# Kernel tuning notes

Hardware: AMD Instinct MI355X
Metric: run time of the kernel (lower is better)

Reference implementation:

```python
import jax, jax.numpy as jnp
import numpy as np

C = 256; G = 16; GC = C // G; K = 3; P = K * K
N = 4; H = 64; W = 64
PAD = 1; OFFSET_SCALE = 1.0; LN_EPS = 1e-5


def setup_inputs() -> dict:
    key = jax.random.key(0)
    ks = jax.random.split(key, 8)
    s = 0.02
    return {
        "x": jax.random.normal(ks[0], (N, C, H, W), jnp.float32),
        "dw_w": jax.random.normal(ks[1], (C, 1, K, K), jnp.float32) * s,
        "dw_b": jnp.zeros((C,), jnp.float32),
        "ln_g": jnp.ones((C,), jnp.float32),
        "ln_b": jnp.zeros((C,), jnp.float32),
        "off_w": jax.random.normal(ks[2], (C, G * P * 2), jnp.float32) * s,
        "off_b": jnp.zeros((G * P * 2,), jnp.float32),
        "mask_w": jax.random.normal(ks[3], (C, G * P), jnp.float32) * s,
        "mask_b": jnp.zeros((G * P,), jnp.float32),
        "inp_w": jax.random.normal(ks[4], (C, C), jnp.float32) * s,
        "inp_b": jnp.zeros((C,), jnp.float32),
        "out_w": jax.random.normal(ks[5], (C, C), jnp.float32) * s,
        "out_b": jnp.zeros((C,), jnp.float32),
    }


def _dcnv3_nchw(x, dw_w, dw_b, ln_g, ln_b, off_w, off_b, mask_w, mask_b,
                inp_w, inp_b, out_w, out_b):
    # NCHW -> NHWC (wrapper permute)
    xn = jnp.transpose(x, (0, 2, 3, 1))                      # (N,H,W,C)
    x_proj = xn @ inp_w + inp_b                              # input_proj

    # offset/mask branch: depthwise conv (NCHW) -> LayerNorm (channels-last) -> GELU
    x1 = jax.lax.conv_general_dilated(
        x, dw_w, window_strides=(1, 1), padding=((PAD, PAD), (PAD, PAD)),
        dimension_numbers=("NCHW", "OIHW", "NCHW"), feature_group_count=C)
    x1 = jnp.transpose(x1, (0, 2, 3, 1)) + dw_b
    mu = x1.mean(-1, keepdims=True)
    var = ((x1 - mu) ** 2).mean(-1, keepdims=True)
    x1 = (x1 - mu) * jax.lax.rsqrt(var + LN_EPS) * ln_g + ln_b
    x1 = jax.nn.gelu(x1, approximate=False)

    offset = (x1 @ off_w + off_b).reshape(N, H, W, G, P, 2)  # (x,y) pairs
    mask = jax.nn.softmax((x1 @ mask_w + mask_b).reshape(N, H, W, G, P), axis=-1)

    # pad sampled feature map with zeros (F.pad before sampling)
    xp = jnp.pad(x_proj, ((0, 0), (PAD, PAD), (PAD, PAD), (0, 0)))
    Hin, Win = H + 2 * PAD, W + 2 * PAD
    xg = xp.reshape(N, Hin, Win, G, GC)

    # reference points, normalized by padded size
    ref_y = (jnp.arange(H, dtype=jnp.float32) + PAD + 0.5) / Hin
    ref_x = (jnp.arange(W, dtype=jnp.float32) + PAD + 0.5) / Win
    ref = jnp.stack([jnp.broadcast_to(ref_x[None, :], (H, W)),
                     jnp.broadcast_to(ref_y[:, None], (H, W))], -1)  # (H,W,2)

    # dilation grid: x varies in the outer loop (torch meshgrid 'ij')
    d = jnp.arange(K, dtype=jnp.float32) - (K - 1) // 2     # [-1,0,1]
    gx = jnp.repeat(d, K) / Win
    gy = jnp.tile(d, K) / Hin
    grid = jnp.stack([gx, gy], -1)                           # (P,2)

    norm = jnp.array([Win, Hin], jnp.float32)
    loc = (ref[None, :, :, None, None, :] + grid * OFFSET_SCALE
           + offset * OFFSET_SCALE / norm)                   # (N,H,W,G,P,2)

    # grid_sample bilinear, align_corners=False, zero padding
    px = loc[..., 0] * Win - 0.5
    py = loc[..., 1] * Hin - 0.5
    x0 = jnp.floor(px); y0 = jnp.floor(py)
    wx = px - x0; wy = py - y0
    x0i = x0.astype(jnp.int32); y0i = y0.astype(jnp.int32)

    n_idx = jnp.arange(N)[:, None, None, None, None]
    g_idx = jnp.arange(G)[None, None, None, :, None]

    def corner(iy, ix, w):
        valid = (iy >= 0) & (iy < Hin) & (ix >= 0) & (ix < Win)
        v = xg[n_idx, jnp.clip(iy, 0, Hin - 1), jnp.clip(ix, 0, Win - 1), g_idx]
        wgt = jnp.where(valid, w, 0.0) * mask                # fold mask into weights
        return jnp.einsum("nhwgp,nhwgpc->nhwgc", wgt, v)

    out = (corner(y0i, x0i, (1 - wy) * (1 - wx))
           + corner(y0i, x0i + 1, (1 - wy) * wx)
           + corner(y0i + 1, x0i, wy * (1 - wx))
           + corner(y0i + 1, x0i + 1, wy * wx))               # (N,H,W,G,GC)

    out = out.reshape(N, H, W, C) @ out_w + out_b            # output_proj
    return jnp.transpose(out, (0, 3, 1, 2))                  # NHWC -> NCHW


def reference(x, dw_w, dw_b, ln_g, ln_b, off_w, off_b, mask_w, mask_b,
              inp_w, inp_b, out_w, out_b):
    return _dcnv3_nchw(x, dw_w, dw_b, ln_g, ln_b, off_w, off_b,
                       mask_w, mask_b, inp_w, inp_b, out_w, out_b)
```

## Files before the change

kernel.cpp:

```cpp
#include <hip/hip_runtime.h>
#include <hip/hip_bf16.h>
#include <math.h>


using bf16x8 = __attribute__((ext_vector_type(8))) short;
using f32x4  = __attribute__((ext_vector_type(4))) float;

#define GLOBAL_AS __attribute__((address_space(1)))
#define LDS_AS    __attribute__((address_space(3)))

static __device__ inline void g2lds16(const void* g, void* l) {
  __builtin_amdgcn_global_load_lds((const GLOBAL_AS int*)g, (LDS_AS int*)l, 16, 0, 0);
}
static __device__ inline unsigned short f2bf(float v) {
  __hip_bfloat16 b = __float2bfloat16(v);
  return *reinterpret_cast<unsigned short*>(&b);
}
static __device__ inline float us2f(unsigned short u) {
  union { unsigned u; float f; } c; c.u = ((unsigned)u) << 16; return c.f;
}

__global__ __launch_bounds__(256) void prep_k(
    const float* __restrict__ inp_w, const float* __restrict__ off_w,
    const float* __restrict__ off_b, const float* __restrict__ mask_w,
    const float* __restrict__ mask_b, const float* __restrict__ out_w,
    __hip_bfloat16* __restrict__ BtI, __hip_bfloat16* __restrict__ BtOM,
    __hip_bfloat16* __restrict__ BtO, float* __restrict__ bOM)
{
  int b = blockIdx.x, t = threadIdx.x;
  if (b < 256) {
    int n = b;
    BtI[n * 256 + t] = __float2bfloat16(inp_w[t * 256 + n]);
  } else if (b < 768) {
    int n = b - 256;
    float v = 0.f;
    if (n < 288) v = off_w[t * 288 + n];
    else if (n < 432) v = mask_w[t * 144 + (n - 288)];
    BtOM[n * 256 + t] = __float2bfloat16(v);
    if (b == 256) {
      for (int idx = t; idx < 512; idx += 256) {
        float bv = (idx < 288) ? off_b[idx] : ((idx < 432) ? mask_b[idx - 288] : 0.f);
        bOM[idx] = bv;
      }
    }
  } else {
    int n = b - 768;
    BtO[n * 256 + t] = __float2bfloat16(out_w[t * 256 + n]);
  }
}

__global__ __launch_bounds__(1024) void stage2_k(
    const float* __restrict__ x,
    const float* __restrict__ dw_w, const float* __restrict__ dw_b,
    const float* __restrict__ ln_g, const float* __restrict__ ln_b,
    const __hip_bfloat16* __restrict__ BtI, const float* __restrict__ inp_b,
    const __hip_bfloat16* __restrict__ BtOM, const float* __restrict__ bOM,
    __hip_bfloat16* __restrict__ xpu, __hip_bfloat16* __restrict__ om)
{
  __shared__ __align__(16) char smem[65152];
  unsigned short* x1t = (unsigned short*)smem;
  unsigned short* xs  = (unsigned short*)(smem + 33792);
  short* BsI  = (short*)(smem + 33792 + 13824);
  float* wgt  = (float*)(smem + 64000);
  float* psq  = (float*)(smem + 33792);
  float* murs = (float*)(smem + 64000);
  short* BsOM = (short*)(smem + 33792);

  const int blk = blockIdx.x;
  const int n4 = blk >> 6, h = blk & 63;
  const int t = threadIdx.x;
  const int w = t & 63, q = t >> 6;

  const int wave = t >> 6, lane = t & 63;
  const int quad = lane >> 4, lr = lane & 15;
  const int wm = wave >> 2, wn = wave & 3;

  f32x4 acc_i[4];
  #pragma unroll
  for (int i = 0; i < 4; ++i) acc_i[i] = (f32x4){0.f, 0.f, 0.f, 0.f};

  float s1 = 0.f, s2 = 0.f;
  for (int chunk = 0; chunk < 8; ++chunk) {
    const int ch0 = chunk * 32;
    if (t < 768) {
      int seg = t >> 3, part = t & 7;
      int r = seg >> 5, c = seg & 31;
      int px0 = part * 8;
      int hh = h + r - 1;
      float4 v0 = {0,0,0,0}, v1 = {0,0,0,0};
      if ((unsigned)hh < 64u) {
        const float* src = x + (size_t)n4 * 1048576 + (size_t)(ch0 + c) * 4096 + hh * 64 + px0;
        v0 = *(const float4*)src;
        v1 = *(const float4*)(src + 4);
      }
      uint4 u;
      u.x = (unsigned)f2bf(v0.x) | ((unsigned)f2bf(v0.y) << 16);
      u.y = (unsigned)f2bf(v0.z) | ((unsigned)f2bf(v0.w) << 16);
      u.z = (unsigned)f2bf(v1.x) | ((unsigned)f2bf(v1.y) << 16);
      u.w = (unsigned)f2bf(v1.z) | ((unsigned)f2bf(v1.w) << 16);
      *(uint4*)&xs[(r * 32 + c) * 72 + px0] = u;
    }
    if (t < 288) {
      int p = t >> 5, lc = t & 31;
      wgt[p * 32 + lc] = dw_w[(ch0 + lc) * 9 + p];
    }
    g2lds16(BtI + (size_t)(t >> 2) * 256 + ch0 + (t & 3) * 8, (char*)BsI + t * 16);
    __syncthreads();
    {
      int lc = 2 * q;
      int c = ch0 + lc;
      float a0 = dw_b[c], a1 = dw_b[c + 1];
      #pragma unroll
      for (int p = 0; p < 9; ++p) {
        int dh = p / 3, dwd = p % 3 - 1;
        int ww = w + dwd;
        if ((unsigned)ww < 64u) {
          float wa = wgt[p * 32 + lc], wb = wgt[p * 32 + lc + 1];
          a0 = fmaf(us2f(xs[(dh * 32 + lc) * 72 + ww]), wa, a0);
          a1 = fmaf(us2f(xs[(dh * 32 + lc + 1) * 72 + ww]), wb, a1);
        }
      }
      s1 += a0 + a1;
      s2 = fmaf(a0, a0, fmaf(a1, a1, s2));
      *(unsigned*)&x1t[w * 264 + c] = (unsigned)f2bf(a0) | ((unsigned)f2bf(a1) << 16);
    }
    {
      bf16x8 af;
      #pragma unroll
      for (int j = 0; j < 8; ++j)
        ((unsigned short*)&af)[j] = xs[(32 + quad * 8 + j) * 72 + wm * 16 + lr];
      #pragma unroll
      for (int ni = 0; ni < 4; ++ni) {
        bf16x8 bf = *(const bf16x8*)&BsI[(wn * 64 + ni * 16 + lr) * 32 + quad * 8];
        acc_i[ni] = __builtin_amdgcn_mfma_f32_16x16x32_bf16(af, bf, acc_i[ni], 0, 0, 0);
      }
    }
    __syncthreads();
  }

  const size_t pix0 = (size_t)n4 * 4096 + (size_t)h * 64;
  #pragma unroll
  for (int ni = 0; ni < 4; ++ni) {
    int col = wn * 64 + ni * 16 + lr;
    float bv = inp_b[col];
    #pragma unroll
    for (int reg = 0; reg < 4; ++reg) {
      int m = wm * 16 + quad * 4 + reg;
      xpu[(pix0 + m) * 256 + col] = __float2bfloat16(acc_i[ni][reg] + bv);
    }
  }

  psq[q * 64 + w] = s1;
  psq[1024 + q * 64 + w] = s2;
  __syncthreads();
  if (t < 64) {
    float a = 0.f, b = 0.f;
    #pragma unroll
    for (int j = 0; j < 16; ++j) { a += psq[j * 64 + t]; b += psq[1024 + j * 64 + t]; }
    float mu = a * (1.f / 256.f);
    murs[t] = mu;
    murs[64 + t] = rsqrtf(b * (1.f / 256.f) - mu * mu + 1e-5f);
  }
  __syncthreads();
  {
    float mu = murs[w], rs = murs[64 + w];
    #pragma unroll
    for (int chunk = 0; chunk < 8; ++chunk) {
      int c = chunk * 32 + 2 * q;
      unsigned pk = *(const unsigned*)&x1t[w * 264 + c];
      float v0 = us2f((unsigned short)(pk & 0xffff));
      float v1 = us2f((unsigned short)(pk >> 16));
      float y0 = fmaf((v0 - mu) * rs, ln_g[c], ln_b[c]);
      float y1 = fmaf((v1 - mu) * rs, ln_g[c + 1], ln_b[c + 1]);
      float g0 = 0.5f * y0 * (1.f + erff(y0 * 0.70710678f));
      float g1 = 0.5f * y1 * (1.f + erff(y1 * 0.70710678f));
      *(unsigned*)&x1t[w * 264 + c] = (unsigned)f2bf(g0) | ((unsigned)f2bf(g1) << 16);
    }
  }

  f32x4 acc[7];
  #pragma unroll
  for (int i = 0; i < 7; ++i) acc[i] = (f32x4){0.f, 0.f, 0.f, 0.f};

  for (int kt = 0; kt < 256; kt += 32) {
    __syncthreads();
    {
      int col = t >> 2, kq = t & 3;
      g2lds16(BtOM + (size_t)col * 256 + kt + kq * 8, (char*)BsOM + t * 16);
      int j = t + 1024;
      if (j < 1792) {
        col = j >> 2; kq = j & 3;
        g2lds16(BtOM + (size_t)col * 256 + kt + kq * 8, (char*)BsOM + j * 16);
      }
    }
    __syncthreads();
    bf16x8 af = *(const bf16x8*)&x1t[(wm * 16 + lr) * 264 + kt + quad * 8];
    #pragma unroll
    for (int ni = 0; ni < 7; ++ni) {
      bf16x8 bf = *(const bf16x8*)&BsOM[(wn * 112 + ni * 16 + lr) * 32 + quad * 8];
      acc[ni] = __builtin_amdgcn_mfma_f32_16x16x32_bf16(af, bf, acc[ni], 0, 0, 0);
    }
  }

  #pragma unroll
  for (int ni = 0; ni < 7; ++ni) {
    int col = wn * 112 + ni * 16 + lr;
    if (col < 432) {
      float bv = bOM[col];
      #pragma unroll
      for (int reg = 0; reg < 4; ++reg) {
        int m = wm * 16 + quad * 4 + reg;
        om[(pix0 + m) * 448 + col] = __float2bfloat16(acc[ni][reg] + bv);
      }
    }
  }
}

__global__ __launch_bounds__(256) void samp_o(
    const __hip_bfloat16* __restrict__ xpu, const __hip_bfloat16* __restrict__ om,
    const __hip_bfloat16* __restrict__ BtO, const float* __restrict__ out_b,
    float* __restrict__ out)
{
  __shared__ __align__(16) char smem[39168];
  unsigned short* oms   = (unsigned short*)smem;
  unsigned short* sampS = (unsigned short*)(smem + 14336);
  short* Bs = (short*)(smem + 22784);
  float* tb = (float*)smem;

  const int bid = blockIdx.x;
  const int region = bid & 7;
  const int qb = bid >> 3;
  const int pix0 = region * 2048 + qb * 16;
  const int n4 = pix0 >> 12, hw0 = pix0 & 4095;
  const int t = threadIdx.x;

  {
    const uint4* gsrc = (const uint4*)(om + (size_t)pix0 * 448);
    uint4* ldst = (uint4*)oms;
    #pragma unroll
    for (int r = 0; r < 4; ++r) {
      int i = t + r * 256;
      if (i < 896) ldst[i] = gsrc[i];
    }
  }
  __syncthreads();

  {
    const int g = t & 15;
    const int pl = t >> 4;
    const int hw = hw0 + pl;
    const int h = hw >> 6, w = hw & 63;

    float mk[9];
    const unsigned short* mp = &oms[pl * 448 + 288 + g * 9];
    float mx = -1e30f;
    #pragma unroll
    for (int p = 0; p < 9; ++p) { mk[p] = us2f(mp[p]); mx = fmaxf(mx, mk[p]); }
    float se = 0.f;
    #pragma unroll
    for (int p = 0; p < 9; ++p) { mk[p] = __expf(mk[p] - mx); se += mk[p]; }
    float inv = 1.f / se;
    #pragma unroll
    for (int p = 0; p < 9; ++p) mk[p] *= inv;

    const unsigned short* op = &oms[pl * 448 + g * 18];
    const __hip_bfloat16* xpg = xpu + (g << 4);
    float ax[16];
    #pragma unroll
    for (int i = 0; i < 16; ++i) ax[i] = 0.f;

    auto corner = [&](int iy, int ix, float wt) {
      if ((unsigned)(iy - 1) >= 64u || (unsigned)(ix - 1) >= 64u) return;
      const __hip_bfloat16* src =
          xpg + ((size_t)((n4 << 12) + (iy - 1) * 64 + (ix - 1)) << 8);
      uint4 u0 = *(const uint4*)src;
      uint4 u1 = *(const uint4*)(src + 8);
      const unsigned uu[8] = {u0.x, u0.y, u0.z, u0.w, u1.x, u1.y, u1.z, u1.w};
      #pragma unroll
      for (int i = 0; i < 8; ++i) {
        float lo = us2f((unsigned short)(uu[i] & 0xffff));
        float hi = us2f((unsigned short)(uu[i] >> 16));
        ax[2 * i + 0] = fmaf(wt, lo, ax[2 * i + 0]);
        ax[2 * i + 1] = fmaf(wt, hi, ax[2 * i + 1]);
      }
    };

    #pragma unroll
    for (int p = 0; p < 9; ++p) {
      float ox = us2f(op[2 * p]), oy = us2f(op[2 * p + 1]);
      float px = (float)(w + p / 3) + ox;
      float py = (float)(h + p % 3) + oy;
      float xf = floorf(px), yf = floorf(py);
      float wx = px - xf, wy = py - yf;
      int ix = (int)xf, iy = (int)yf;
      float m = mk[p];
      corner(iy,     ix,     (1.f - wy) * (1.f - wx) * m);
      corner(iy,     ix + 1, (1.f - wy) * wx * m);
      corner(iy + 1, ix,     wy * (1.f - wx) * m);
      corner(iy + 1, ix + 1, wy * wx * m);
    }

    unsigned short ub[16];
    #pragma unroll
    for (int i = 0; i < 16; ++i) ub[i] = f2bf(ax[i]);
    uint4 u0, u1;
    u0.x = (unsigned)ub[0] | ((unsigned)ub[1] << 16);
    u0.y = (unsigned)ub[2] | ((unsigned)ub[3] << 16);
    u0.z = (unsigned)ub[4] | ((unsigned)ub[5] << 16);
    u0.w = (unsigned)ub[6] | ((unsigned)ub[7] << 16);
    u1.x = (unsigned)ub[8] | ((unsigned)ub[9] << 16);
    u1.y = (unsigned)ub[10] | ((unsigned)ub[11] << 16);
    u1.z = (unsigned)ub[12] | ((unsigned)ub[13] << 16);
    u1.w = (unsigned)ub[14] | ((unsigned)ub[15] << 16);
    *(uint4*)&sampS[pl * 264 + g * 16] = u0;
    *(uint4*)&sampS[pl * 264 + g * 16 + 8] = u1;
  }
  __syncthreads();

  const int wave = t >> 6, lane = t & 63;
  const int quad = lane >> 4, lr = lane & 15;
  f32x4 acc[4];
  #pragma unroll
  for (int i = 0; i < 4; ++i) acc[i] = (f32x4){0.f, 0.f, 0.f, 0.f};

  for (int kt = 0; kt < 256; kt += 32) {
    if (kt) __syncthreads();
    #pragma unroll
    for (int j = 0; j < 4; ++j) {
      int idx = j * 256 + t;
      int col = idx >> 2, kq = idx & 3;
      g2lds16(BtO + (size_t)col * 256 + kt + kq * 8, (char*)Bs + idx * 16);
    }
    __syncthreads();
    bf16x8 af = *(const bf16x8*)&sampS[lr * 264 + kt + quad * 8];
    #pragma unroll
    for (int ni = 0; ni < 4; ++ni) {
      bf16x8 bf = *(const bf16x8*)&Bs[(wave * 64 + ni * 16 + lr) * 32 + quad * 8];
      acc[ni] = __builtin_amdgcn_mfma_f32_16x16x32_bf16(af, bf, acc[ni], 0, 0, 0);
    }
  }
  __syncthreads();

  #pragma unroll
  for (int ni = 0; ni < 4; ++ni) {
    int col = wave * 64 + ni * 16 + lr;
    float bv = out_b[col];
    #pragma unroll
    for (int reg = 0; reg < 4; ++reg)
      tb[col * 17 + quad * 4 + reg] = acc[ni][reg] + bv;
  }
  __syncthreads();

  {
    int co = t;
    float* dst = out + (size_t)(n4 * 256 + co) * 4096 + hw0;
    #pragma unroll
    for (int j = 0; j < 4; ++j) {
      float4 v;
      v.x = tb[co * 17 + j * 4 + 0];
      v.y = tb[co * 17 + j * 4 + 1];
      v.z = tb[co * 17 + j * 4 + 2];
      v.w = tb[co * 17 + j * 4 + 3];
      *(float4*)(dst + j * 4) = v;
    }
  }
}

extern "C" void kernel_launch(void* const* d_in, const int* in_sizes, int n_in,
                              void* d_out, int out_size, void* d_ws, size_t ws_size,
                              hipStream_t stream) {
  const float* x      = (const float*)d_in[0];
  const float* dw_w   = (const float*)d_in[1];
  const float* dw_b   = (const float*)d_in[2];
  const float* ln_g   = (const float*)d_in[3];
  const float* ln_b   = (const float*)d_in[4];
  const float* off_w  = (const float*)d_in[5];
  const float* off_b  = (const float*)d_in[6];
  const float* mask_w = (const float*)d_in[7];
  const float* mask_b = (const float*)d_in[8];
  const float* inp_w  = (const float*)d_in[9];
  const float* inp_b  = (const float*)d_in[10];
  const float* out_w  = (const float*)d_in[11];
  const float* out_b  = (const float*)d_in[12];
  float* out = (float*)d_out;

  char* w0 = (char*)d_ws;
  __hip_bfloat16* xpu  = (__hip_bfloat16*)(w0);
  __hip_bfloat16* om   = (__hip_bfloat16*)(w0 + 8388608);
  __hip_bfloat16* BtI  = (__hip_bfloat16*)(w0 + 23068672);
  __hip_bfloat16* BtOM = (__hip_bfloat16*)(w0 + 23199744);
  __hip_bfloat16* BtO  = (__hip_bfloat16*)(w0 + 23461888);
  float*          bOM  = (float*)(w0 + 23592960);
  if (ws_size < 23595008) return;

  prep_k<<<1024, 256, 0, stream>>>(inp_w, off_w, off_b, mask_w, mask_b, out_w,
                                   BtI, BtOM, BtO, bOM);
  stage2_k<<<256, 1024, 0, stream>>>(x, dw_w, dw_b, ln_g, ln_b, BtI, inp_b,
                                     BtOM, bOM, xpu, om);
  samp_o<<<1024, 256, 0, stream>>>(xpu, om, BtO, out_b, out);
}
```

Before: 164.9 us.

## Split stage2 into half-row blocks with register-prefetched double-buffered input

Each stage2 block now handles 32 pixels instead of 64, giving 512 blocks of 512 threads and a smaller LDS footprint so more blocks fit per CU. The x tile for the next channel chunk is loaded into registers while the current chunk computes, then stored into a second LDS buffer. Weight matrices BtI and BtOM are read directly from global/L2 instead of being staged through LDS, which removes a pair of barriers per K-step. In exchange, depthwise halo columns are loaded redundantly and the MFMA B operands depend on cache hits.

Measured after the change: 186.1 us. 1.13x slower.

```diff
diff --git a/kernel.cpp b/kernel.cpp
--- a/kernel.cpp
+++ b/kernel.cpp
@@ -18,6 +18,9 @@
 }
 static __device__ inline float us2f(unsigned short u) {
   union { unsigned u; float f; } c; c.u = ((unsigned)u) << 16; return c.f;
+}
+static __device__ inline unsigned pk2(float a, float b) {
+  return (unsigned)f2bf(a) | ((unsigned)f2bf(b) << 16);
 }
 
 __global__ __launch_bounds__(256) void prep_k(
@@ -49,7 +52,7 @@
   }
 }
 
-__global__ __launch_bounds__(1024) void stage2_k(
+__global__ __launch_bounds__(512, 6) void stage2_k(
     const float* __restrict__ x,
     const float* __restrict__ dw_w, const float* __restrict__ dw_b,
     const float* __restrict__ ln_g, const float* __restrict__ ln_b,
@@ -57,88 +60,111 @@
     const __hip_bfloat16* __restrict__ BtOM, const float* __restrict__ bOM,
     __hip_bfloat16* __restrict__ xpu, __hip_bfloat16* __restrict__ om)
 {
-  __shared__ __align__(16) char smem[65152];
+  __shared__ __align__(16) char smem[46080];
   unsigned short* x1t = (unsigned short*)smem;
-  unsigned short* xs  = (unsigned short*)(smem + 33792);
-  short* BsI  = (short*)(smem + 33792 + 13824);
-  float* wgt  = (float*)(smem + 64000);
-  float* psq  = (float*)(smem + 33792);
-  float* murs = (float*)(smem + 64000);
-  short* BsOM = (short*)(smem + 33792);
+  unsigned short* xs  = (unsigned short*)(smem + 16896);
+  float* wgt  = (float*)(smem + 36864);
+  float* psq  = (float*)(smem + 16896);
+  float* murs = (float*)(smem + 20992);
 
   const int blk = blockIdx.x;
-  const int n4 = blk >> 6, h = blk & 63;
+  const int n4 = blk >> 7, h = (blk >> 1) & 63;
+  const int px0 = (blk & 1) * 32;
   const int t = threadIdx.x;
-  const int w = t & 63, q = t >> 6;
-
+  const int w = t & 31, q = t >> 5;
   const int wave = t >> 6, lane = t & 63;
   const int quad = lane >> 4, lr = lane & 15;
   const int wm = wave >> 2, wn = wave & 3;
 
+  for (int i = t; i < 2304; i += 512) {
+    float v = dw_w[i];
+    wgt[(i % 9) * 256 + (i / 9)] = v;
+  }
+
+  int r0, c0, lpx0, gpx0, r1, c1, lpx1, gpx1;
+  {
+    int id = t;
+    r0 = id / 192; int rem = id - r0 * 192; c0 = rem / 6; int cp = rem - c0 * 6;
+    lpx0 = cp * 8; gpx0 = px0 - 8 + lpx0;
+  }
+  const bool tb2 = (t < 64);
+  if (tb2) {
+    int id = 512 + t;
+    r1 = id / 192; int rem = id - r1 * 192; c1 = rem / 6; int cp = rem - c1 * 6;
+    lpx1 = cp * 8; gpx1 = px0 - 8 + lpx1;
+  }
+
+  auto ldx = [&](int chunk, int r, int c, int gpx, float4& a, float4& b) {
+    a = make_float4(0.f, 0.f, 0.f, 0.f);
+    b = make_float4(0.f, 0.f, 0.f, 0.f);
+    int hh = h + r - 1;
+    if ((unsigned)hh < 64u && (unsigned)gpx < 57u) {
+      const float* s = x + (size_t)n4 * 1048576 + (size_t)(chunk * 32 + c) * 4096 + hh * 64 + gpx;
+      a = *(const float4*)s;
+      b = *(const float4*)(s + 4);
+    }
+  };
+  auto stx = [&](int buf, int r, int c, int lpx, float4 a, float4 b) {
+    unsigned short* d = &xs[buf * 4992 + (r * 32 + c) * 52 + lpx];
+    uint2 u0, u1;
+    u0.x = pk2(a.x, a.y); u0.y = pk2(a.z, a.w);
+    u1.x = pk2(b.x, b.y); u1.y = pk2(b.z, b.w);
+    *(uint2*)d = u0; *(uint2*)(d + 4) = u1;
+  };
+
   f32x4 acc_i[4];
   #pragma unroll
   for (int i = 0; i < 4; ++i) acc_i[i] = (f32x4){0.f, 0.f, 0.f, 0.f};
+
+  float4 pa0, pb0, pa1, pb1;
+  ldx(0, r0, c0, gpx0, pa0, pb0);
+  if (tb2) ldx(0, r1, c1, gpx1, pa1, pb1);
+  stx(0, r0, c0, lpx0, pa0, pb0);
+  if (tb2) stx(0, r1, c1, lpx1, pa1, pb1);
+  __syncthreads();
 
   float s1 = 0.f, s2 = 0.f;
   for (int chunk = 0; chunk < 8; ++chunk) {
+    const int buf = chunk & 1;
     const int ch0 = chunk * 32;
-    if (t < 768) {
-      int seg = t >> 3, part = t & 7;
-      int r = seg >> 5, c = seg & 31;
-      int px0 = part * 8;
-      int hh = h + r - 1;
-      float4 v0 = {0,0,0,0}, v1 = {0,0,0,0};
-      if ((unsigned)hh < 64u) {
-        const float* src = x + (size_t)n4 * 1048576 + (size_t)(ch0 + c) * 4096 + hh * 64 + px0;
-        v0 = *(const float4*)src;
-        v1 = *(const float4*)(src + 4);
-      }
-      uint4 u;
-      u.x = (unsigned)f2bf(v0.x) | ((unsigned)f2bf(v0.y) << 16);
-      u.y = (unsigned)f2bf(v0.z) | ((unsigned)f2bf(v0.w) << 16);
-      u.z = (unsigned)f2bf(v1.x) | ((unsigned)f2bf(v1.y) << 16);
-      u.w = (unsigned)f2bf(v1.z) | ((unsigned)f2bf(v1.w) << 16);
-      *(uint4*)&xs[(r * 32 + c) * 72 + px0] = u;
-    }
-    if (t < 288) {
-      int p = t >> 5, lc = t & 31;
-      wgt[p * 32 + lc] = dw_w[(ch0 + lc) * 9 + p];
-    }
-    g2lds16(BtI + (size_t)(t >> 2) * 256 + ch0 + (t & 3) * 8, (char*)BsI + t * 16);
-    __syncthreads();
+    if (chunk < 7) {
+      ldx(chunk + 1, r0, c0, gpx0, pa0, pb0);
+      if (tb2) ldx(chunk + 1, r1, c1, gpx1, pa1, pb1);
+    }
+    const unsigned short* xb = &xs[buf * 4992];
     {
-      int lc = 2 * q;
-      int c = ch0 + lc;
+      int lc = 2 * q, c = ch0 + lc;
       float a0 = dw_b[c], a1 = dw_b[c + 1];
       #pragma unroll
       for (int p = 0; p < 9; ++p) {
         int dh = p / 3, dwd = p % 3 - 1;
-        int ww = w + dwd;
-        if ((unsigned)ww < 64u) {
-          float wa = wgt[p * 32 + lc], wb = wgt[p * 32 + lc + 1];
-          a0 = fmaf(us2f(xs[(dh * 32 + lc) * 72 + ww]), wa, a0);
-          a1 = fmaf(us2f(xs[(dh * 32 + lc + 1) * 72 + ww]), wb, a1);
-        }
+        int ii = 8 + w + dwd;
+        a0 = fmaf(us2f(xb[(dh * 32 + lc) * 52 + ii]), wgt[p * 256 + c], a0);
+        a1 = fmaf(us2f(xb[(dh * 32 + lc + 1) * 52 + ii]), wgt[p * 256 + c + 1], a1);
       }
       s1 += a0 + a1;
       s2 = fmaf(a0, a0, fmaf(a1, a1, s2));
-      *(unsigned*)&x1t[w * 264 + c] = (unsigned)f2bf(a0) | ((unsigned)f2bf(a1) << 16);
+      *(unsigned*)&x1t[w * 264 + c] = pk2(a0, a1);
     }
     {
       bf16x8 af;
       #pragma unroll
       for (int j = 0; j < 8; ++j)
-        ((unsigned short*)&af)[j] = xs[(32 + quad * 8 + j) * 72 + wm * 16 + lr];
+        ((unsigned short*)&af)[j] = xb[(32 + quad * 8 + j) * 52 + 8 + wm * 16 + lr];
       #pragma unroll
       for (int ni = 0; ni < 4; ++ni) {
-        bf16x8 bf = *(const bf16x8*)&BsI[(wn * 64 + ni * 16 + lr) * 32 + quad * 8];
+        bf16x8 bf = *(const bf16x8*)&BtI[(size_t)(wn * 64 + ni * 16 + lr) * 256 + ch0 + quad * 8];
         acc_i[ni] = __builtin_amdgcn_mfma_f32_16x16x32_bf16(af, bf, acc_i[ni], 0, 0, 0);
       }
     }
+    if (chunk < 7) {
+      stx(buf ^ 1, r0, c0, lpx0, pa0, pb0);
+      if (tb2) stx(buf ^ 1, r1, c1, lpx1, pa1, pb1);
+    }
     __syncthreads();
   }
 
-  const size_t pix0 = (size_t)n4 * 4096 + (size_t)h * 64;
+  const size_t pixb = (size_t)n4 * 4096 + (size_t)h * 64 + px0;
   #pragma unroll
   for (int ni = 0; ni < 4; ++ni) {
     int col = wn * 64 + ni * 16 + lr;
@@ -146,62 +172,50 @@
     #pragma unroll
     for (int reg = 0; reg < 4; ++reg) {
       int m = wm * 16 + quad * 4 + reg;
-      xpu[(pix0 + m) * 256 + col] = __float2bfloat16(acc_i[ni][reg] + bv);
-    }
-  }
-
-  psq[q * 64 + w] = s1;
-  psq[1024 + q * 64 + w] = s2;
-  __syncthreads();
-  if (t < 64) {
+      xpu[(pixb + m) * 256 + col] = __float2bfloat16(acc_i[ni][reg] + bv);
+    }
+  }
+
+  psq[q * 32 + w] = s1;
+  psq[512 + q * 32 + w] = s2;
+  __syncthreads();
+  if (t < 32) {
     float a = 0.f, b = 0.f;
     #pragma unroll
-    for (int j = 0; j < 16; ++j) { a += psq[j * 64 + t]; b += psq[1024 + j * 64 + t]; }
+    for (int j = 0; j < 16; ++j) { a += psq[j * 32 + t]; b += psq[512 + j * 32 + t]; }
     float mu = a * (1.f / 256.f);
     murs[t] = mu;
-    murs[64 + t] = rsqrtf(b * (1.f / 256.f) - mu * mu + 1e-5f);
+    murs[32 + t] = rsqrtf(b * (1.f / 256.f) - mu * mu + 1e-5f);
   }
   __syncthreads();
   {
-    float mu = murs[w], rs = murs[64 + w];
+    float mu = murs[w], rs = murs[32 + w];
     #pragma unroll
     for (int chunk = 0; chunk < 8; ++chunk) {
       int c = chunk * 32 + 2 * q;
-      unsigned pk = *(const unsigned*)&x1t[w * 264 + c];
-      float v0 = us2f((unsigned short)(pk & 0xffff));
-      float v1 = us2f((unsigned short)(pk >> 16));
+      unsigned pkv = *(const unsigned*)&x1t[w * 264 + c];
+      float v0 = us2f((unsigned short)(pkv & 0xffff));
+      float v1 = us2f((unsigned short)(pkv >> 16));
       float y0 = fmaf((v0 - mu) * rs, ln_g[c], ln_b[c]);
       float y1 = fmaf((v1 - mu) * rs, ln_g[c + 1], ln_b[c + 1]);
       float g0 = 0.5f * y0 * (1.f + erff(y0 * 0.70710678f));
       float g1 = 0.5f * y1 * (1.f + erff(y1 * 0.70710678f));
-      *(unsigned*)&x1t[w * 264 + c] = (unsigned)f2bf(g0) | ((unsigned)f2bf(g1) << 16);
-    }
-  }
+      *(unsigned*)&x1t[w * 264 + c] = pk2(g0, g1);
+    }
+  }
+  __syncthreads();
 
   f32x4 acc[7];
   #pragma unroll
   for (int i = 0; i < 7; ++i) acc[i] = (f32x4){0.f, 0.f, 0.f, 0.f};
-
   for (int kt = 0; kt < 256; kt += 32) {
-    __syncthreads();
-    {
-      int col = t >> 2, kq = t & 3;
-      g2lds16(BtOM + (size_t)col * 256 + kt + kq * 8, (char*)BsOM + t * 16);
-      int j = t + 1024;
-      if (j < 1792) {
-        col = j >> 2; kq = j & 3;
-        g2lds16(BtOM + (size_t)col * 256 + kt + kq * 8, (char*)BsOM + j * 16);
-      }
-    }
-    __syncthreads();
     bf16x8 af = *(const bf16x8*)&x1t[(wm * 16 + lr) * 264 + kt + quad * 8];
     #pragma unroll
     for (int ni = 0; ni < 7; ++ni) {
-      bf16x8 bf = *(const bf16x8*)&BsOM[(wn * 112 + ni * 16 + lr) * 32 + quad * 8];
+      bf16x8 bf = *(const bf16x8*)&BtOM[(size_t)(wn * 112 + ni * 16 + lr) * 256 + kt + quad * 8];
       acc[ni] = __builtin_amdgcn_mfma_f32_16x16x32_bf16(af, bf, acc[ni], 0, 0, 0);
     }
   }
-
   #pragma unroll
   for (int ni = 0; ni < 7; ++ni) {
     int col = wn * 112 + ni * 16 + lr;
@@ -210,7 +224,7 @@
       #pragma unroll
       for (int reg = 0; reg < 4; ++reg) {
         int m = wm * 16 + quad * 4 + reg;
-        om[(pix0 + m) * 448 + col] = __float2bfloat16(acc[ni][reg] + bv);
+        om[(pixb + m) * 448 + col] = __float2bfloat16(acc[ni][reg] + bv);
       }
     }
   }
@@ -395,7 +409,7 @@
 
   prep_k<<<1024, 256, 0, stream>>>(inp_w, off_w, off_b, mask_w, mask_b, out_w,
                                    BtI, BtOM, BtO, bOM);
-  stage2_k<<<256, 1024, 0, stream>>>(x, dw_w, dw_b, ln_g, ln_b, BtI, inp_b,
-                                     BtOM, bOM, xpu, om);
+  stage2_k<<<512, 512, 0, stream>>>(x, dw_w, dw_b, ln_g, ln_b, BtI, inp_b,
+                                    BtOM, bOM, xpu, om);
   samp_o<<<1024, 256, 0, stream>>>(xpu, om, BtO, out_b, out);
 }
```
